# Kernel tuning notes

Hardware: AMD Instinct MI355X
Metric: run time of the kernel (lower is better)

Reference implementation:

```python
import jax, jax.numpy as jnp
import numpy as np

V_IN, V_OUT = 32000, 32000
E, H = 512, 1024
B, S, T = 64, 128, 64


def setup_inputs() -> dict:
    key = jax.random.key(0)
    ks = jax.random.split(key, 13)
    s = 0.05
    return {
        "src": jax.random.randint(ks[0], (B, S), 0, V_IN, dtype=jnp.int32),
        "trg": jax.random.randint(ks[1], (B, T), 0, V_OUT, dtype=jnp.int32),
        "tf_mask": jax.random.randint(ks[2], (T,), 0, 2, dtype=jnp.int32),
        "enc_emb": jax.random.normal(ks[3], (V_IN, E), jnp.float32) * s,
        "dec_emb": jax.random.normal(ks[4], (V_OUT, E), jnp.float32) * s,
        "Wih_e": jax.random.normal(ks[5], (4 * H, E), jnp.float32) * s,
        "Whh_e": jax.random.normal(ks[6], (4 * H, H), jnp.float32) * s,
        "b_e": jax.random.normal(ks[7], (4 * H,), jnp.float32) * s,
        "Wih_d": jax.random.normal(ks[8], (4 * H, E), jnp.float32) * s,
        "Whh_d": jax.random.normal(ks[9], (4 * H, H), jnp.float32) * s,
        "b_d": jax.random.normal(ks[10], (4 * H,), jnp.float32) * s,
        "Wfc": jax.random.normal(ks[11], (V_OUT, H), jnp.float32) * s,
        "bfc": jax.random.normal(ks[12], (V_OUT,), jnp.float32) * s,
    }


def lstm_step(h, c, x, Wih, Whh, b):
    # PyTorch LSTM gate order: input, forget, cell(g), output
    g = x @ Wih.T + h @ Whh.T + b  # [B, 4H]
    i, f, gg, o = jnp.split(g, 4, axis=-1)
    c_new = jax.nn.sigmoid(f) * c + jax.nn.sigmoid(i) * jnp.tanh(gg)
    h_new = jax.nn.sigmoid(o) * jnp.tanh(c_new)
    return h_new, c_new


def reference(src, trg, tf_mask, enc_emb, dec_emb, Wih_e, Whh_e, b_e,
              Wih_d, Whh_d, b_d, Wfc, bfc):
    b, t_len = trg.shape
    dt = Wfc.dtype
    hdim = Whh_e.shape[1]

    # ----- Encoder (dropout is identity in eval mode) -----
    x_src = enc_emb[src]  # [B, S, E]
    h0 = jnp.zeros((b, hdim), dt)
    c0 = jnp.zeros((b, hdim), dt)

    def enc_step(carry, x_t):
        h, c = carry
        h, c = lstm_step(h, c, x_t, Wih_e, Whh_e, b_e)
        return (h, c), None

    (h, c), _ = jax.lax.scan(enc_step, (h0, c0), jnp.swapaxes(x_src, 0, 1))

    # ----- Decoder loop over t = 1 .. T-1 -----
    def dec_step(carry, xs):
        h, c, inp = carry
        trg_t, tf = xs
        x = dec_emb[inp]  # [B, E]
        h, c = lstm_step(h, c, x, Wih_d, Whh_d, b_d)
        logits = h @ Wfc.T + bfc  # [B, V]
        nxt = jnp.where(tf > 0, trg_t, jnp.argmax(logits, axis=-1).astype(trg_t.dtype))
        return (h, c, nxt), logits

    xs = (jnp.swapaxes(trg, 0, 1)[1:], tf_mask[1:])
    _, logits = jax.lax.scan(dec_step, (h, c, trg[:, 0]), xs)  # [T-1, B, V]

    # outputs[:, 0, :] stays zeros, as in the original
    out = jnp.concatenate([jnp.zeros((1, b, logits.shape[-1]), logits.dtype), logits], axis=0)
    return jnp.swapaxes(out, 0, 1)  # [B, T, V]
```

## Files before the change

kernel.cpp:

```cpp
#include <hip/hip_runtime.h>
#include <math.h>

#define Hd 1024
#define Ed 512
#define Bv 64
#define Sv 128
#define Tv 64
#define Vv 32000
#define NB 256

typedef __attribute__((ext_vector_type(8))) short bf16x8;
typedef __attribute__((ext_vector_type(4))) float f32x4;
typedef unsigned long long ull;

__device__ __forceinline__ float sigf(float x){ return 1.0f/(1.0f + expf(-x)); }
__device__ __forceinline__ unsigned short f2bf(float f){
  unsigned u = __float_as_uint(f);
  return (unsigned short)((u + 0x7FFFu + ((u>>16)&1u)) >> 16);
}
__device__ __forceinline__ float bf2f(unsigned short b){ return __uint_as_float(((unsigned)b)<<16); }
__device__ __forceinline__ void split3(float v, unsigned short& s0, unsigned short& s1, unsigned short& s2){
  s0 = f2bf(v);
  float r1 = v - bf2f(s0);
  s1 = f2bf(r1);
  s2 = f2bf(r1 - bf2f(s1));
}
#define MF(A,B,C) __builtin_amdgcn_mfma_f32_16x16x32_bf16(A,B,C,0,0,0)

#define OFF_H    65536
#define H_PL     4259840L
#define OFF_WE   6455296
#define OFF_WD   15892480
#define W_PL     6291456L
#define OFF_WF   25329664
#define WF_PL    32768000L
#define OFF_TOK  58097664
#define OFF_CNT  58105728
#define NEED_FL  58106240


__global__ __launch_bounds__(256) void k_wsplit3(
    const float* __restrict__ Wih, const float* __restrict__ Whh,
    unsigned short* __restrict__ d0, unsigned short* __restrict__ d1, unsigned short* __restrict__ d2)
{
  const int n = blockIdx.x;
  const int tid = threadIdx.x;
  const int g = n >> 10, jt = (n & 1023) >> 4, nl = n & 15;
  const long base = ((long)(g*64 + jt)*48) << 9;
  #pragma unroll
  for (int i = 0; i < 6; ++i){
    int k = tid + 256*i;
    float v = (k < 512) ? Wih[(long)n*512 + k] : Whh[(long)n*1024 + (k-512)];
    int kt = k >> 5, lk = (k >> 3) & 3, ke = k & 7;
    long dst = base + ((long)kt << 9) + ((lk*16 + nl) << 3) + ke;
    unsigned short s0,s1,s2; split3(v, s0,s1,s2);
    d0[dst] = s0; d1[dst] = s1; d2[dst] = s2;
  }
}

__global__ __launch_bounds__(256) void k_wfsplit(
    const float* __restrict__ W, unsigned short* __restrict__ dhi, unsigned short* __restrict__ dlo)
{
  const int v = blockIdx.x;
  const int tid = threadIdx.x;
  const int vt = v >> 4, vl = v & 15;
  const long base = ((long)vt*32) << 9;
  #pragma unroll
  for (int i = 0; i < 4; ++i){
    int k = tid + 256*i;
    float x = W[(long)v*1024 + k];
    int kt = k >> 5, lk = (k >> 3) & 3, ke = k & 7;
    long dst = base + ((long)kt << 9) + ((lk*16 + vl) << 3) + ke;
    unsigned short h = f2bf(x);
    dhi[dst] = h;
    dlo[dst] = f2bf(x - bf2f(h));
  }
}

__device__ __forceinline__ void gbar(int* cnt, int idx){
  __syncthreads();
  if (threadIdx.x == 0){
    __hip_atomic_fetch_add(&cnt[idx], 1, __ATOMIC_RELEASE, __HIP_MEMORY_SCOPE_AGENT);
    while (__hip_atomic_load(&cnt[idx], __ATOMIC_RELAXED, __HIP_MEMORY_SCOPE_AGENT) < NB)
      __builtin_amdgcn_s_sleep(2);
    __builtin_amdgcn_fence(__ATOMIC_ACQUIRE, "workgroup");
  }
  __syncthreads();
}

template<bool DEC>
__device__ __forceinline__ void lstm_phase(
    int b, int tid, int slot_in, int slot_out, int tj,
    const unsigned short* __restrict__ W0s, const unsigned short* __restrict__ W1s,
    const unsigned short* __restrict__ W2s, const float* __restrict__ bias,
    const int* __restrict__ tok_src, const int* __restrict__ tf,
    const float* __restrict__ emb, const ull* __restrict__ toku,
    unsigned short* __restrict__ H, float* __restrict__ c,
    float (*g4)[16][16], short (*hst)[16][16], int* stok)
{
  const int g = tid >> 6, lane = tid & 63;
  const int l15 = lane & 15, lk = lane >> 4;
  const int jh = (b & 63) * 16;
  const int m0 = (b >> 6) * 16;
  const int mt = b >> 6;
  const long wbase = ((long)(g*64 + (b & 63))*48) << 9;
  const unsigned short* w0 = W0s + wbase;
  const unsigned short* w1 = W1s + wbase;
  const unsigned short* w2 = W2s + wbase;
  const unsigned short* h0 = H + (long)slot_in*65536;
  const unsigned short* h1 = h0 + H_PL;
  const unsigned short* h2 = h0 + 2*H_PL;

  if (tid < 16){
    int m = m0 + tid, tk;
    if (!DEC){
      tk = tok_src[m*Sv + tj];
    } else {
      if (tj == 0) tk = tok_src[m*Tv];
      else if (tf[tj] > 0) tk = tok_src[m*Tv + tj];
      else tk = (int)(~(unsigned)__hip_atomic_load(&toku[(long)(tj-1)*64 + m],
                     __ATOMIC_RELAXED, __HIP_MEMORY_SCOPE_AGENT));
    }
    stok[tid] = tk;
  }
  __syncthreads();

  f32x4 acc = (f32x4){0.f,0.f,0.f,0.f};

  {
    const float* e0 = emb + (long)stok[l15]*Ed;
    #pragma unroll 2
    for (int kt = 0; kt < 16; ++kt){
      const int k0 = kt*32 + lk*8;
      bf16x8 b0  = *(const bf16x8*)(w0 + ((long)kt << 9) + (lane << 3));
      bf16x8 b1v = *(const bf16x8*)(w1 + ((long)kt << 9) + (lane << 3));
      bf16x8 b2  = *(const bf16x8*)(w2 + ((long)kt << 9) + (lane << 3));
      bf16x8 a0,a1,a2;
      float4 pa = *(const float4*)(e0 + k0);
      float4 pb = *(const float4*)(e0 + k0 + 4);
      float fv[8] = {pa.x,pa.y,pa.z,pa.w,pb.x,pb.y,pb.z,pb.w};
      #pragma unroll
      for (int e=0;e<8;++e){ unsigned short s0,s1,s2; split3(fv[e],s0,s1,s2);
        a0[e]=(short)s0; a1[e]=(short)s1; a2[e]=(short)s2; }
      acc = MF(a0,b0,acc); acc = MF(a1,b0,acc); acc = MF(a0,b1v,acc);
      acc = MF(a2,b0,acc); acc = MF(a0,b2,acc); acc = MF(a1,b1v,acc);
    }
  }
  {
    #pragma unroll 2
    for (int kt = 0; kt < 32; ++kt){
      bf16x8 b0  = *(const bf16x8*)(w0 + ((long)(16+kt) << 9) + (lane << 3));
      bf16x8 b1v = *(const bf16x8*)(w1 + ((long)(16+kt) << 9) + (lane << 3));
      bf16x8 b2  = *(const bf16x8*)(w2 + ((long)(16+kt) << 9) + (lane << 3));
      const long ho = (((long)mt*32 + kt) << 9) + (lane << 3);
      bf16x8 a0 = *(const bf16x8*)(h0 + ho);
      bf16x8 a1 = *(const bf16x8*)(h1 + ho);
      bf16x8 a2 = *(const bf16x8*)(h2 + ho);
      acc = MF(a0,b0,acc); acc = MF(a1,b0,acc); acc = MF(a0,b1v,acc);
      acc = MF(a2,b0,acc); acc = MF(a0,b2,acc); acc = MF(a1,b1v,acc);
    }
  }

  #pragma unroll
  for (int r = 0; r < 4; ++r) g4[g][lk*4 + r][l15] = acc[r];
  __syncthreads();

  {
    const int mloc = tid >> 4, cl = tid & 15;
    const int col = jh + cl;
    float ig = g4[0][mloc][cl] + bias[col];
    float fg = g4[1][mloc][cl] + bias[Hd + col];
    float gg = g4[2][mloc][cl] + bias[2*Hd + col];
    float og = g4[3][mloc][cl] + bias[3*Hd + col];
    long idx = (long)(m0 + mloc)*Hd + col;
    float cv = c[idx];
    float cn = sigf(fg)*cv + sigf(ig)*tanhf(gg);
    float hn = sigf(og)*tanhf(cn);
    c[idx] = cn;
    unsigned short s0,s1,s2; split3(hn, s0,s1,s2);
    hst[0][mloc][cl] = (short)s0; hst[1][mloc][cl] = (short)s1; hst[2][mloc][cl] = (short)s2;
  }
  __syncthreads();
  if (tid < 192){
    const int p = tid >> 6, t2 = tid & 63, r = t2 >> 2, q = t2 & 3;
    ull v =
        (ull)(unsigned short)hst[p][r][q*4]
      | ((ull)(unsigned short)hst[p][r][q*4+1] << 16)
      | ((ull)(unsigned short)hst[p][r][q*4+2] << 32)
      | ((ull)(unsigned short)hst[p][r][q*4+3] << 48);
    const int kt = (b & 63) >> 1;
    const int off16 = (jh & 16) + q*4;
    const int lkw = off16 >> 3, keb = off16 & 7;
    ull* dst = (ull*)(H + (long)p*H_PL + (long)slot_out*65536
                      + (((long)mt*32 + kt) << 9) + ((lkw*16 + r) << 3) + keb);
    __hip_atomic_store(dst, v, __ATOMIC_RELAXED, __HIP_MEMORY_SCOPE_AGENT);
  }
}

__device__ __forceinline__ void fc_phase(
    int b, int tid,
    const unsigned short* __restrict__ hhi, const unsigned short* __restrict__ hlo,
    const unsigned short* __restrict__ Wfhi, const unsigned short* __restrict__ Wflo,
    const float* __restrict__ bfc,
    ull* __restrict__ tslot, ull* amax)
{
  if (tid < 64) amax[tid] = 0ULL;
  __syncthreads();
  const int wv = tid >> 6, lane = tid & 63;
  const int l15 = lane & 15, lk = lane >> 4;
  const int vt0 = b*8 + wv*2;
  const int v0 = vt0*16 + l15, v1 = (vt0+1)*16 + l15;

  f32x4 acc[2][4];
  #pragma unroll
  for (int nv=0; nv<2; ++nv)
    #pragma unroll
    for (int mt=0; mt<4; ++mt) acc[nv][mt] = (f32x4){0.f,0.f,0.f,0.f};

  #pragma unroll 2
  for (int kt = 0; kt < 32; ++kt){
    const long wo0 = (((long)vt0*32 + kt) << 9) + (lane << 3);
    const long wo1 = (((long)(vt0+1)*32 + kt) << 9) + (lane << 3);
    bf16x8 bh0 = *(const bf16x8*)(Wfhi + wo0);
    bf16x8 bl0 = *(const bf16x8*)(Wflo + wo0);
    bf16x8 bh1 = *(const bf16x8*)(Wfhi + wo1);
    bf16x8 bl1 = *(const bf16x8*)(Wflo + wo1);
    #pragma unroll
    for (int mt=0; mt<4; ++mt){
      const long ho = (((long)mt*32 + kt) << 9) + (lane << 3);
      bf16x8 ah = *(const bf16x8*)(hhi + ho);
      bf16x8 al = *(const bf16x8*)(hlo + ho);
      acc[0][mt] = MF(ah, bh0, acc[0][mt]);
      acc[0][mt] = MF(al, bh0, acc[0][mt]);
      acc[0][mt] = MF(ah, bl0, acc[0][mt]);
      acc[1][mt] = MF(ah, bh1, acc[1][mt]);
      acc[1][mt] = MF(al, bh1, acc[1][mt]);
      acc[1][mt] = MF(ah, bl1, acc[1][mt]);
    }
  }
  float bb0 = bfc[v0], bb1 = bfc[v1];
  #pragma unroll
  for (int mt=0; mt<4; ++mt){
    #pragma unroll
    for (int r=0; r<4; ++r){
      int m = mt*16 + lk*4 + r;
      float f0 = acc[0][mt][r] + bb0;
      float f1 = acc[1][mt][r] + bb1;
      unsigned u0 = __float_as_uint(f0); u0 ^= (u0 >> 31) ? 0xFFFFFFFFu : 0x80000000u;
      unsigned u1 = __float_as_uint(f1); u1 ^= (u1 >> 31) ? 0xFFFFFFFFu : 0x80000000u;
      ull c0 = ((ull)u0 << 32) | (unsigned)(~v0);
      ull c1 = ((ull)u1 << 32) | (unsigned)(~v1);
      ull cm = c0 > c1 ? c0 : c1;
      #pragma unroll
      for (int d=1; d<16; d<<=1){
        ull o = __shfl_xor(cm, d);
        if (o > cm) cm = o;
      }
      if (l15 == 0) atomicMax(&amax[m], cm);
    }
  }
  __syncthreads();
  if (tid < 64) atomicMax(tslot + tid, amax[tid]);
}

__global__ __launch_bounds__(256, 1) void k_mega(
    const int* __restrict__ src, const int* __restrict__ trg, const int* __restrict__ tf,
    const float* __restrict__ enc_emb, const float* __restrict__ dec_emb,
    const float* __restrict__ b_e, const float* __restrict__ b_d,
    const float* __restrict__ bfc,
    float* __restrict__ ws)
{
  __shared__ float g4[4][16][16];
  __shared__ short hst[3][16][16];
  __shared__ int stok[16];
  __shared__ ull amax[64];

  const int b = blockIdx.x, tid = threadIdx.x;
  float* c = ws;
  unsigned short* H = (unsigned short*)(ws + OFF_H);
  const unsigned short* We0 = (const unsigned short*)(ws + OFF_WE);
  const unsigned short* We1 = We0 + W_PL;
  const unsigned short* We2 = We0 + 2*W_PL;
  const unsigned short* Wd0 = (const unsigned short*)(ws + OFF_WD);
  const unsigned short* Wd1 = Wd0 + W_PL;
  const unsigned short* Wd2 = Wd0 + 2*W_PL;
  const unsigned short* Wfhi = (const unsigned short*)(ws + OFF_WF);
  const unsigned short* Wflo = Wfhi + WF_PL;
  ull* toku = (ull*)(ws + OFF_TOK);
  int* cnt = (int*)(ws + OFF_CNT);
  int bar = 0;

  {
    const int jh = (b & 63)*16, m0 = (b >> 6)*16;
    const int mloc = tid >> 4, cl = tid & 15;
    c[(long)(m0+mloc)*Hd + jh + cl] = 0.f;
    if (tid < 96){
      long off_ull = (long)b*96 + tid;
      int p = (int)(off_ull >> 13);
      long q = off_ull & 8191;
      ull* dst = (ull*)(H + (long)p*H_PL + 64L*65536) + q;
      __hip_atomic_store(dst, 0ULL, __ATOMIC_RELAXED, __HIP_MEMORY_SCOPE_AGENT);
    }
  }
  gbar(cnt, bar++);

  for (int t = 0; t < Sv; ++t){
    lstm_phase<false>(b, tid, 63 + ((t+1)&1), 63 + (t&1), t,
        We0, We1, We2, b_e, src, (const int*)0, enc_emb,
        (const ull*)0, H, c, g4, hst, stok);
    gbar(cnt, bar++);
  }
  for (int j = 0; j < Tv-1; ++j){
    lstm_phase<true>(b, tid, (j == 0) ? 64 : (j-1), j, j,
        Wd0, Wd1, Wd2, b_d, trg, tf, dec_emb, toku, H, c, g4, hst, stok);
    gbar(cnt, bar++);
    if (j < Tv-2 && tf[j+1] == 0){
      if (b < 250){
        const unsigned short* h0 = H + (long)j*65536;
        fc_phase(b, tid, h0, h0 + H_PL, Wfhi, Wflo, bfc, toku + (long)j*64, amax);
      }
      gbar(cnt, bar++);
    }
  }
}

__global__ __launch_bounds__(256) void k_fcall(
    const unsigned short* __restrict__ Wfhi, const unsigned short* __restrict__ Wflo,
    const float* __restrict__ bfc,
    const unsigned short* __restrict__ H, float* __restrict__ out)
{
  const int tid = threadIdx.x;
  const int wv = tid >> 6, lane = tid & 63;
  const int l15 = lane & 15, lk = lane >> 4;
  const int vt = blockIdx.x*4 + wv;
  const int vcol = vt*16 + l15;
  const int jbase = blockIdx.y*4;
  const unsigned short* h0b = H + (long)jbase*65536;
  const unsigned short* h1b = h0b + H_PL;

  f32x4 acc[4][4];
  #pragma unroll
  for (int jj=0;jj<4;++jj)
    #pragma unroll
    for (int mt=0;mt<4;++mt) acc[jj][mt] = (f32x4){0.f,0.f,0.f,0.f};

  for (int kt = 0; kt < 32; ++kt){
    const long wo = (((long)vt*32 + kt) << 9) + (lane << 3);
    bf16x8 bh = *(const bf16x8*)(Wfhi + wo);
    bf16x8 bl = *(const bf16x8*)(Wflo + wo);
    #pragma unroll
    for (int jj=0;jj<4;++jj){
      if (jbase + jj <= 62){
        #pragma unroll
        for (int mt=0;mt<4;++mt){
          const long ho = (long)jj*65536 + (((long)mt*32 + kt) << 9) + (lane << 3);
          bf16x8 ah = *(const bf16x8*)(h0b + ho);
          bf16x8 al = *(const bf16x8*)(h1b + ho);
          acc[jj][mt] = MF(ah, bh, acc[jj][mt]);
          acc[jj][mt] = MF(al, bh, acc[jj][mt]);
          acc[jj][mt] = MF(ah, bl, acc[jj][mt]);
        }
      }
    }
  }
  float bb = bfc[vcol];
  #pragma unroll
  for (int jj=0;jj<4;++jj){
    if (jbase + jj <= 62){
      #pragma unroll
      for (int mt=0;mt<4;++mt){
        #pragma unroll
        for (int r=0;r<4;++r){
          int m = mt*16 + lk*4 + r;
          out[((long)m*Tv + (jbase+jj+1))*(long)Vv + vcol] = acc[jj][mt][r] + bb;
        }
      }
    }
  }
  if (blockIdx.y == 0){
    const int vb = blockIdx.x*64;
    for (int i = tid; i < 4096; i += 256){
      int m = i >> 6, v = vb + (i & 63);
      out[(long)m*Tv*(long)Vv + v] = 0.f;
    }
  }
}


__global__ __launch_bounds__(256) void k_initC(float* __restrict__ ws, float* __restrict__ out){
  long i = (long)blockIdx.x*256 + threadIdx.x;
  if (i < 262144){ ws[i] = 0.f; }
  else {
    long r = i - 262144;
    long m = r / Vv, v = r % Vv;
    out[m*Tv*(long)Vv + v] = 0.f;
  }
}

__global__ __launch_bounds__(256) void k_stepC(
    int mode, int t,
    const int* __restrict__ tok_src, const int* __restrict__ tf_mask,
    const int* __restrict__ token_buf, const float* __restrict__ emb,
    const float* __restrict__ Wih, const float* __restrict__ Whh,
    const float* __restrict__ bias,
    const float* __restrict__ h_in, const float* __restrict__ c_in,
    float* __restrict__ h_out, float* __restrict__ c_out,
    unsigned short* __restrict__ hsp_hi, unsigned short* __restrict__ hsp_lo)
{
  __shared__ __align__(16) float tile[8*1536];
  __shared__ float gbuf[4*8*32];
  __shared__ int toks[8];
  const int tid = threadIdx.x;
  const int m0 = blockIdx.y*8, jh0 = blockIdx.x*32;
  if (tid < 8){
    int m = m0 + tid; int tok;
    if (mode == 0) tok = tok_src[m*Sv + t];
    else { if (t == 0) tok = tok_src[m*Tv];
           else tok = (tf_mask[t] > 0) ? tok_src[m*Tv + t] : token_buf[m]; }
    toks[tid] = tok;
  }
  __syncthreads();
  { float4* t4 = (float4*)tile;
    #pragma unroll
    for (int r = 0; r < 12; ++r){
      int f = tid + 256*r; int row = f / 384, o = f % 384; float4 v;
      if (o < 128) v = ((const float4*)(emb + (long)toks[row]*Ed))[o];
      else         v = ((const float4*)(h_in + (long)(m0+row)*Hd))[o-128];
      t4[row*384 + o] = v; } }
  __syncthreads();
  const int g = tid >> 6, sx = tid & 63, jl = sx & 31, mg = sx >> 5;
  const int col = g*Hd + jh0 + jl;
  const float4* wx = (const float4*)(Wih + (long)col*Ed);
  const float4* wh = (const float4*)(Whh + (long)col*Hd);
  const float4* t4 = (const float4*)tile;
  const int mb = mg*4;
  float bq = bias[col];
  float a0=bq, a1=bq, a2=bq, a3=bq;
  for (int k = 0; k < 128; ++k){
    float4 w = wx[k];
    float4 v0 = t4[(mb+0)*384 + k]; float4 v1 = t4[(mb+1)*384 + k];
    float4 v2 = t4[(mb+2)*384 + k]; float4 v3 = t4[(mb+3)*384 + k];
    a0 += w.x*v0.x + w.y*v0.y + w.z*v0.z + w.w*v0.w;
    a1 += w.x*v1.x + w.y*v1.y + w.z*v1.z + w.w*v1.w;
    a2 += w.x*v2.x + w.y*v2.y + w.z*v2.z + w.w*v2.w;
    a3 += w.x*v3.x + w.y*v3.y + w.z*v3.z + w.w*v3.w;
  }
  for (int k = 0; k < 256; ++k){
    float4 w = wh[k];
    float4 v0 = t4[(mb+0)*384 + 128 + k]; float4 v1 = t4[(mb+1)*384 + 128 + k];
    float4 v2 = t4[(mb+2)*384 + 128 + k]; float4 v3 = t4[(mb+3)*384 + 128 + k];
    a0 += w.x*v0.x + w.y*v0.y + w.z*v0.z + w.w*v0.w;
    a1 += w.x*v1.x + w.y*v1.y + w.z*v1.z + w.w*v1.w;
    a2 += w.x*v2.x + w.y*v2.y + w.z*v2.z + w.w*v2.w;
    a3 += w.x*v3.x + w.y*v3.y + w.z*v3.z + w.w*v3.w;
  }
  gbuf[g*256 + (mb+0)*32 + jl] = a0; gbuf[g*256 + (mb+1)*32 + jl] = a1;
  gbuf[g*256 + (mb+2)*32 + jl] = a2; gbuf[g*256 + (mb+3)*32 + jl] = a3;
  __syncthreads();
  const int ml = tid >> 5, j2 = tid & 31;
  float ig = gbuf[0*256 + ml*32 + j2];
  float fg = gbuf[1*256 + ml*32 + j2];
  float gg = gbuf[2*256 + ml*32 + j2];
  float og = gbuf[3*256 + ml*32 + j2];
  long idx = (long)(m0+ml)*Hd + jh0 + j2;
  float cc = c_in[idx];
  float cn = sigf(fg)*cc + sigf(ig)*tanhf(gg);
  float hn = sigf(og)*tanhf(cn);
  c_out[idx] = cn; h_out[idx] = hn;
  unsigned short hh = f2bf(hn);
  hsp_hi[idx] = hh; hsp_lo[idx] = f2bf(hn - bf2f(hh));
}

__global__ __launch_bounds__(256) void k_fcC(
    int j, const unsigned short* __restrict__ hhi, const unsigned short* __restrict__ hlo,
    const float* __restrict__ Wfc, const float* __restrict__ bfc, float* __restrict__ out)
{
  const int tid = threadIdx.x;
  const int wv = tid >> 6, lane = tid & 63;
  const int l15 = lane & 15, lk = lane >> 4;
  const int vcol = blockIdx.x*64 + wv*16 + l15;
  const float* wrow = Wfc + (long)vcol*Hd;
  f32x4 acc[4];
  #pragma unroll
  for (int mt=0; mt<4; ++mt) acc[mt] = (f32x4){0.f,0.f,0.f,0.f};
  #pragma unroll 2
  for (int kt = 0; kt < 32; ++kt){
    const int k0 = kt*32 + lk*8;
    float4 wa = *(const float4*)(wrow + k0);
    float4 wb = *(const float4*)(wrow + k0 + 4);
    float wf[8] = {wa.x,wa.y,wa.z,wa.w,wb.x,wb.y,wb.z,wb.w};
    bf16x8 bh, bl;
    #pragma unroll
    for (int e=0;e<8;++e){
      unsigned short h = f2bf(wf[e]);
      bh[e] = (short)h; bl[e] = (short)f2bf(wf[e] - bf2f(h));
    }
    #pragma unroll
    for (int mt=0; mt<4; ++mt){
      const int row = mt*16 + l15;
      bf16x8 ah = *(const bf16x8*)(hhi + row*Hd + k0);
      bf16x8 al = *(const bf16x8*)(hlo + row*Hd + k0);
      acc[mt] = MF(ah, bh, acc[mt]);
      acc[mt] = MF(al, bh, acc[mt]);
      acc[mt] = MF(ah, bl, acc[mt]);
    }
  }
  float bb = bfc[vcol];
  #pragma unroll
  for (int mt=0; mt<4; ++mt)
    #pragma unroll
    for (int r=0; r<4; ++r){
      int m = mt*16 + lk*4 + r;
      out[((long)m*Tv + (j+1))*(long)Vv + vcol] = acc[mt][r] + bb;
    }
}

__global__ __launch_bounds__(256) void k_argmaxC(
    int j, const float* __restrict__ out, int* __restrict__ token_buf)
{
  __shared__ float sval[256];
  __shared__ int   sidx[256];
  const int m = blockIdx.x, tid = threadIdx.x;
  const float* base = out + ((long)m*Tv + (j+1))*(long)Vv;
  float best = -INFINITY; int bi = 0;
  for (int v = tid; v < Vv; v += 256){
    float f = base[v];
    if (f > best){ best = f; bi = v; }
  }
  sval[tid] = best; sidx[tid] = bi;
  __syncthreads();
  for (int s2 = 128; s2 > 0; s2 >>= 1){
    if (tid < s2){
      float ov = sval[tid+s2]; int oi = sidx[tid+s2];
      if (ov > sval[tid] || (ov == sval[tid] && oi < sidx[tid])){
        sval[tid] = ov; sidx[tid] = oi;
      }
    }
    __syncthreads();
  }
  if (tid == 0) token_buf[m] = sidx[0];
}

extern "C" void kernel_launch(void* const* d_in, const int* in_sizes, int n_in,
                              void* d_out, int out_size, void* d_ws, size_t ws_size,
                              hipStream_t stream)
{
  const int*   src     = (const int*)  d_in[0];
  const int*   trg     = (const int*)  d_in[1];
  const int*   tf      = (const int*)  d_in[2];
  const float* enc_emb = (const float*)d_in[3];
  const float* dec_emb = (const float*)d_in[4];
  const float* Wih_e   = (const float*)d_in[5];
  const float* Whh_e   = (const float*)d_in[6];
  const float* b_e     = (const float*)d_in[7];
  const float* Wih_d   = (const float*)d_in[8];
  const float* Whh_d   = (const float*)d_in[9];
  const float* b_d     = (const float*)d_in[10];
  const float* Wfc     = (const float*)d_in[11];
  const float* bfc     = (const float*)d_in[12];
  float* out = (float*)d_out;
  float* ws  = (float*)d_ws;

  if (ws_size >= (size_t)NEED_FL * 4ULL){
    unsigned short* We0 = (unsigned short*)(ws + OFF_WE);
    unsigned short* Wd0 = (unsigned short*)(ws + OFF_WD);
    unsigned short* Wf0 = (unsigned short*)(ws + OFF_WF);
    unsigned short* Hb  = (unsigned short*)(ws + OFF_H);

    hipMemsetAsync((void*)(ws + OFF_TOK), 0, (size_t)(NEED_FL - OFF_TOK) * 4ULL, stream);
    k_wsplit3<<<4096, 256, 0, stream>>>(Wih_e, Whh_e, We0, We0 + W_PL, We0 + 2*W_PL);
    k_wsplit3<<<4096, 256, 0, stream>>>(Wih_d, Whh_d, Wd0, Wd0 + W_PL, Wd0 + 2*W_PL);
    k_wfsplit<<<32000, 256, 0, stream>>>(Wfc, Wf0, Wf0 + WF_PL);
    k_mega<<<NB, 256, 0, stream>>>(src, trg, tf, enc_emb, dec_emb, b_e, b_d, bfc, ws);
    k_fcall<<<dim3(500, 16), 256, 0, stream>>>(Wf0, Wf0 + WF_PL, bfc, Hb, out);
  } else {
    float* hbuf[2] = { ws,            ws + 65536 };
    float* cbuf[2] = { ws + 131072,   ws + 196608 };
    int*   tokbuf  = (int*)(ws + 262144);
    unsigned short* hsp_hi = (unsigned short*)(ws + 262208);
    unsigned short* hsp_lo = (unsigned short*)(ws + 262208 + 32768);

    k_initC<<<9024, 256, 0, stream>>>(ws, out);
    int cur = 0;
    for (int t = 0; t < Sv; ++t){
      k_stepC<<<dim3(32,8), 256, 0, stream>>>(0, t, src, tf, tokbuf, enc_emb,
          Wih_e, Whh_e, b_e, hbuf[cur], cbuf[cur], hbuf[cur^1], cbuf[cur^1], hsp_hi, hsp_lo);
      cur ^= 1;
    }
    for (int j = 0; j < Tv-1; ++j){
      k_stepC<<<dim3(32,8), 256, 0, stream>>>(1, j, trg, tf, tokbuf, dec_emb,
          Wih_d, Whh_d, b_d, hbuf[cur], cbuf[cur], hbuf[cur^1], cbuf[cur^1], hsp_hi, hsp_lo);
      cur ^= 1;
      k_fcC<<<500, 256, 0, stream>>>(j, hsp_hi, hsp_lo, Wfc, bfc, out);
      if (j < Tv-2) k_argmaxC<<<64, 256, 0, stream>>>(j, out, tokbuf);
    }
  }
}
```

Before: 9.084 ms.

## Double persistent grid to 512 blocks, splitting FC argmax work across more blocks

The persistent megakernel grid goes from 256 to 512 blocks with two blocks per CU allowed. Only half of the blocks, chosen by a parity mapping, run the LSTM phases, while all 500 working blocks share the teacher-forcing-off FC/argmax phase, each covering one 16-column vocab tile per wave instead of two. The aim is to spread the FC matvec across more CUs and waves to cut critical-path latency. In exchange, every grid barrier now waits on twice as many blocks, and idle blocks sit at the barrier during the LSTM steps.

```diff
diff --git a/kernel.cpp b/kernel.cpp
--- a/kernel.cpp
+++ b/kernel.cpp
@@ -7,7 +7,7 @@
 #define Sv 128
 #define Tv 64
 #define Vv 32000
-#define NB 256
+#define NB 512
 
 typedef __attribute__((ext_vector_type(8))) short bf16x8;
 typedef __attribute__((ext_vector_type(4))) float f32x4;
@@ -90,7 +90,7 @@
 
 template<bool DEC>
 __device__ __forceinline__ void lstm_phase(
-    int b, int tid, int slot_in, int slot_out, int tj,
+    int lb, int tid, int slot_in, int slot_out, int tj,
     const unsigned short* __restrict__ W0s, const unsigned short* __restrict__ W1s,
     const unsigned short* __restrict__ W2s, const float* __restrict__ bias,
     const int* __restrict__ tok_src, const int* __restrict__ tf,
@@ -100,10 +100,10 @@
 {
   const int g = tid >> 6, lane = tid & 63;
   const int l15 = lane & 15, lk = lane >> 4;
-  const int jh = (b & 63) * 16;
-  const int m0 = (b >> 6) * 16;
-  const int mt = b >> 6;
-  const long wbase = ((long)(g*64 + (b & 63))*48) << 9;
+  const int jh = (lb & 63) * 16;
+  const int m0 = (lb >> 6) * 16;
+  const int mt = lb >> 6;
+  const long wbase = ((long)(g*64 + (lb & 63))*48) << 9;
   const unsigned short* w0 = W0s + wbase;
   const unsigned short* w1 = W1s + wbase;
   const unsigned short* w2 = W2s + wbase;
@@ -188,7 +188,7 @@
       | ((ull)(unsigned short)hst[p][r][q*4+1] << 16)
       | ((ull)(unsigned short)hst[p][r][q*4+2] << 32)
       | ((ull)(unsigned short)hst[p][r][q*4+3] << 48);
-    const int kt = (b & 63) >> 1;
+    const int kt = (lb & 63) >> 1;
     const int off16 = (jh & 16) + q*4;
     const int lkw = off16 >> 3, keb = off16 & 7;
     ull* dst = (ull*)(H + (long)p*H_PL + (long)slot_out*65536
@@ -208,49 +208,37 @@
   __syncthreads();
   const int wv = tid >> 6, lane = tid & 63;
   const int l15 = lane & 15, lk = lane >> 4;
-  const int vt0 = b*8 + wv*2;
-  const int v0 = vt0*16 + l15, v1 = (vt0+1)*16 + l15;
-
-  f32x4 acc[2][4];
-  #pragma unroll
-  for (int nv=0; nv<2; ++nv)
-    #pragma unroll
-    for (int mt=0; mt<4; ++mt) acc[nv][mt] = (f32x4){0.f,0.f,0.f,0.f};
+  const int vt = b*4 + wv;
+  const int v0 = vt*16 + l15;
+
+  f32x4 acc[4];
+  #pragma unroll
+  for (int mt=0; mt<4; ++mt) acc[mt] = (f32x4){0.f,0.f,0.f,0.f};
 
   #pragma unroll 2
   for (int kt = 0; kt < 32; ++kt){
-    const long wo0 = (((long)vt0*32 + kt) << 9) + (lane << 3);
-    const long wo1 = (((long)(vt0+1)*32 + kt) << 9) + (lane << 3);
-    bf16x8 bh0 = *(const bf16x8*)(Wfhi + wo0);
-    bf16x8 bl0 = *(const bf16x8*)(Wflo + wo0);
-    bf16x8 bh1 = *(const bf16x8*)(Wfhi + wo1);
-    bf16x8 bl1 = *(const bf16x8*)(Wflo + wo1);
+    const long wo = (((long)vt*32 + kt) << 9) + (lane << 3);
+    bf16x8 bh = *(const bf16x8*)(Wfhi + wo);
+    bf16x8 bl = *(const bf16x8*)(Wflo + wo);
     #pragma unroll
     for (int mt=0; mt<4; ++mt){
       const long ho = (((long)mt*32 + kt) << 9) + (lane << 3);
       bf16x8 ah = *(const bf16x8*)(hhi + ho);
       bf16x8 al = *(const bf16x8*)(hlo + ho);
-      acc[0][mt] = MF(ah, bh0, acc[0][mt]);
-      acc[0][mt] = MF(al, bh0, acc[0][mt]);
-      acc[0][mt] = MF(ah, bl0, acc[0][mt]);
-      acc[1][mt] = MF(ah, bh1, acc[1][mt]);
-      acc[1][mt] = MF(al, bh1, acc[1][mt]);
-      acc[1][mt] = MF(ah, bl1, acc[1][mt]);
-    }
-  }
-  float bb0 = bfc[v0], bb1 = bfc[v1];
+      acc[mt] = MF(ah, bh, acc[mt]);
+      acc[mt] = MF(al, bh, acc[mt]);
+      acc[mt] = MF(ah, bl, acc[mt]);
+    }
+  }
+  float bb0 = bfc[v0];
   #pragma unroll
   for (int mt=0; mt<4; ++mt){
     #pragma unroll
     for (int r=0; r<4; ++r){
       int m = mt*16 + lk*4 + r;
-      float f0 = acc[0][mt][r] + bb0;
-      float f1 = acc[1][mt][r] + bb1;
+      float f0 = acc[mt][r] + bb0;
       unsigned u0 = __float_as_uint(f0); u0 ^= (u0 >> 31) ? 0xFFFFFFFFu : 0x80000000u;
-      unsigned u1 = __float_as_uint(f1); u1 ^= (u1 >> 31) ? 0xFFFFFFFFu : 0x80000000u;
-      ull c0 = ((ull)u0 << 32) | (unsigned)(~v0);
-      ull c1 = ((ull)u1 << 32) | (unsigned)(~v1);
-      ull cm = c0 > c1 ? c0 : c1;
+      ull cm = ((ull)u0 << 32) | (unsigned)(~v0);
       #pragma unroll
       for (int d=1; d<16; d<<=1){
         ull o = __shfl_xor(cm, d);
@@ -263,7 +251,7 @@
   if (tid < 64) atomicMax(tslot + tid, amax[tid]);
 }
 
-__global__ __launch_bounds__(256, 1) void k_mega(
+__global__ __launch_bounds__(256, 2) void k_mega(
     const int* __restrict__ src, const int* __restrict__ trg, const int* __restrict__ tf,
     const float* __restrict__ enc_emb, const float* __restrict__ dec_emb,
     const float* __restrict__ b_e, const float* __restrict__ b_d,
@@ -276,6 +264,9 @@
   __shared__ ull amax[64];
 
   const int b = blockIdx.x, tid = threadIdx.x;
+  const bool rl = ((b ^ (b >> 8)) & 1) == 0;
+  const int lb = (b < 256) ? (b >> 1) : (128 + ((b - 256) >> 1));
+
   float* c = ws;
   unsigned short* H = (unsigned short*)(ws + OFF_H);
   const unsigned short* We0 = (const unsigned short*)(ws + OFF_WE);
@@ -290,12 +281,12 @@
   int* cnt = (int*)(ws + OFF_CNT);
   int bar = 0;
 
-  {
-    const int jh = (b & 63)*16, m0 = (b >> 6)*16;
+  if (rl){
+    const int jh = (lb & 63)*16, m0 = (lb >> 6)*16;
     const int mloc = tid >> 4, cl = tid & 15;
     c[(long)(m0+mloc)*Hd + jh + cl] = 0.f;
     if (tid < 96){
-      long off_ull = (long)b*96 + tid;
+      long off_ull = (long)lb*96 + tid;
       int p = (int)(off_ull >> 13);
       long q = off_ull & 8191;
       ull* dst = (ull*)(H + (long)p*H_PL + 64L*65536) + q;
@@ -305,17 +296,19 @@
   gbar(cnt, bar++);
 
   for (int t = 0; t < Sv; ++t){
-    lstm_phase<false>(b, tid, 63 + ((t+1)&1), 63 + (t&1), t,
-        We0, We1, We2, b_e, src, (const int*)0, enc_emb,
-        (const ull*)0, H, c, g4, hst, stok);
+    if (rl)
+      lstm_phase<false>(lb, tid, 63 + ((t+1)&1), 63 + (t&1), t,
+          We0, We1, We2, b_e, src, (const int*)0, enc_emb,
+          (const ull*)0, H, c, g4, hst, stok);
     gbar(cnt, bar++);
   }
   for (int j = 0; j < Tv-1; ++j){
-    lstm_phase<true>(b, tid, (j == 0) ? 64 : (j-1), j, j,
-        Wd0, Wd1, Wd2, b_d, trg, tf, dec_emb, toku, H, c, g4, hst, stok);
+    if (rl)
+      lstm_phase<true>(lb, tid, (j == 0) ? 64 : (j-1), j, j,
+          Wd0, Wd1, Wd2, b_d, trg, tf, dec_emb, toku, H, c, g4, hst, stok);
     gbar(cnt, bar++);
     if (j < Tv-2 && tf[j+1] == 0){
-      if (b < 250){
+      if (b < 500){
         const unsigned short* h0 = H + (long)j*65536;
         fc_phase(b, tid, h0, h0 + H_PL, Wfhi, Wflo, bfc, toku + (long)j*64, amax);
       }
```

Measured after the change: 11.85 ms. 30.5% more time.
